# Kernel tuning notes

Hardware: AMD Instinct MI355X
Metric: run time of the kernel (lower is better)

## Reference

```python
import jax, jax.numpy as jnp
import numpy as np

N = 50000  # nodes per ntype (must be equal across ntypes per the module's forward)
E = 400000  # edges per relation

# relation order matches __init__: (src_ntype, dst_ntype)
RELS = [("stock","financial"),("stock","macro"),("stock","news"),("stock","policy"),
        ("financial","macro"),("financial","stock"),("financial","news"),("financial","policy"),
        ("macro","stock"),("macro","financial"),("macro","news"),("macro","policy"),
        ("news","stock"),("news","financial"),("news","macro"),("news","policy"),
        ("policy","stock"),("policy","macro"),("policy","news"),("policy","financial")]
NTYPES = ["stock","financial","macro","news","policy"]


def graph_conv(x_src, src, dst, W, b):
    # DGL GraphConv, norm='both': h = D_in^{-1/2} A D_out^{-1/2} x W + b
    ones = jnp.ones((src.shape[0],), x_src.dtype)
    deg_out = jax.ops.segment_sum(ones, src, num_segments=N)
    norm_s = jax.lax.rsqrt(jnp.maximum(deg_out, 1.0))
    h = x_src * norm_s[:, None]
    if W.shape[0] > W.shape[1]:  # mult W first when in_feats > out_feats
        h = h @ W
        agg = jax.ops.segment_sum(h[src], dst, num_segments=N)
    else:
        agg = jax.ops.segment_sum(h[src], dst, num_segments=N)
        agg = agg @ W
    deg_in = jax.ops.segment_sum(ones, dst, num_segments=N)
    norm_d = jax.lax.rsqrt(jnp.maximum(deg_in, 1.0))
    return agg * norm_d[:, None] + b


def hetero_layer(feats, edges, W_per_rel, b_per_rel):
    # sum-aggregate per destination ntype (aggregate='sum')
    out = {nt: jnp.zeros((N, b_per_rel[0].shape[0]), jnp.float32) for nt in NTYPES}
    for r, (s_nt, d_nt) in enumerate(RELS):
        out[d_nt] = out[d_nt] + graph_conv(feats[s_nt], edges[r, 0], edges[r, 1], W_per_rel[r], b_per_rel[r])
    return out


def setup_inputs() -> dict:
    key = jax.random.key(0)
    ks = jax.random.split(key, 16)
    H, C = 128, 10
    d = {
        "x_stock": jax.random.normal(ks[0], (N, 5), jnp.float32),
        "x_financial": jax.random.normal(ks[1], (N, 16), jnp.float32),
        "x_macro": jax.random.normal(ks[2], (N, 21), jnp.float32),
        "x_news": jax.random.normal(ks[3], (N, 768), jnp.float32),
        "x_policy": jax.random.normal(ks[4], (N, 768), jnp.float32),
        "W1_stock": jax.random.normal(ks[5], (4, 5, H), jnp.float32) * 0.1,
        "W1_financial": jax.random.normal(ks[6], (4, 16, H), jnp.float32) * 0.1,
        "W1_macro": jax.random.normal(ks[7], (4, 21, H), jnp.float32) * 0.1,
        "W1_news": jax.random.normal(ks[8], (4, 768, H), jnp.float32) * 0.02,
        "W1_policy": jax.random.normal(ks[9], (4, 768, H), jnp.float32) * 0.02,
        "b1": jnp.zeros((20, H), jnp.float32),
        "W2": jax.random.normal(ks[10], (20, H, H), jnp.float32) * 0.05,
        "b2": jnp.zeros((20, H), jnp.float32),
        "Wfc": jax.random.normal(ks[11], (H, C), jnp.float32) * 0.05,
        "bfc": jnp.zeros((C,), jnp.float32),
        "edges": jax.random.randint(ks[12], (20, 2, E), 0, N, dtype=jnp.int32),
    }
    return d


def reference(x_stock, x_financial, x_macro, x_news, x_policy,
              W1_stock, W1_financial, W1_macro, W1_news, W1_policy, b1,
              W2, b2, Wfc, bfc, edges):
    feats = {"stock": x_stock, "financial": x_financial, "macro": x_macro,
             "news": x_news, "policy": x_policy}
    # layer-1 weights in relation order (RELS grouped by src ntype, 4 each)
    W1_by_src = {"stock": W1_stock, "financial": W1_financial, "macro": W1_macro,
                 "news": W1_news, "policy": W1_policy}
    W1_list = [W1_by_src[s][r % 4] for r, (s, _) in enumerate(RELS)]
    b1_list = [b1[r] for r in range(20)]
    h1 = hetero_layer(feats, edges, W1_list, b1_list)
    W2_list = [W2[r] for r in range(20)]
    b2_list = [b2[r] for r in range(20)]
    h2 = hetero_layer(h1, edges, W2_list, b2_list)
    # manual cross-ntype accumulation into stock buffer, then divide by #ntypes
    acc = h2["stock"]
    for nt in NTYPES:
        if nt != "stock":
            acc = acc + h2[nt]
    acc = acc / len(NTYPES)
    # dgl.mean_nodes over a single graph -> [1, H]
    m = jnp.mean(acc, axis=0, keepdims=True)
    out = m @ Wfc + bfc
    return (m, out)
```

## Files before the change

kernel.cpp:

```cpp
#include <hip/hip_runtime.h>

#define NN 50000
#define EE 400000

#define CH_H 32768
#define NCH_H 2
#define ESL_H 2
#define EPS_H (EE/ESL_H)
#define I4_H (EPS_H/4)

#define ESL_C 4
#define EPS_C (EE/ESL_C)
#define I4_C (EPS_C/4)

#define CH_D 4096
#define NCH_D 13
#define ESL_D 2
#define EPS_D (EE/ESL_D)
#define I4_D (EPS_D/4)

#define NZ 261
#define ZROWS 192

#define VCH 96

__constant__ int DSTT[20]     = {1,2,3,4, 2,0,3,4, 0,1,3,4, 0,1,2,4, 0,2,3,1};
__constant__ int KIDX[20]     = {0,0,0,0, 1,0,1,1, 1,1,2,2, 2,2,2,3, 3,3,3,3};
__constant__ int DSTREL[5][4] = {{5,8,12,16},{0,9,13,19},{1,4,14,17},{2,6,10,18},{3,7,11,15}};
__constant__ int FEATS[5]     = {5, 16, 21, 768, 768};

#define OFF_HIST 0
#define OFF_CRAW 0
#define OFF_CC4  0
#define OFF_C    4000000
#define OFF_ND   5000000
#define OFF_PART 0
#define OFF_YS   6500000
#define OFF_S    6600000
#define OFF_V    6700000
#define OFF_NS   7000000
#define OFF_DACC 8000000
#define DSLICE   4000000
#define OFF_Y    8000000
#define OFF_MP   8110000
#define TOTAL_ELEMS 16000000

static __device__ __forceinline__ void fma4(float4& a, const float4& x, float w) {
    a.x += w * x.x; a.y += w * x.y; a.z += w * x.z; a.w += w * x.w;
}

__global__ __launch_bounds__(1024) void k_hist(const int* __restrict__ edges, int* __restrict__ hist_part) {
    __shared__ int h[CH_H];
    const int slice = blockIdx.x, chunk = blockIdx.y;
    const int r = blockIdx.z % 20, arr = blockIdx.z / 20;
    for (int i = threadIdx.x; i < CH_H; i += 1024) h[i] = 0;
    __syncthreads();
    const int4* key = (const int4*)(edges + (size_t)(r*2 + arr)*EE + slice*EPS_H);
    const int base = chunk * CH_H;
    for (int i = threadIdx.x; i < I4_H; i += 1024) {
        int4 k4 = key[i];
        unsigned a = (unsigned)(k4.x - base), b = (unsigned)(k4.y - base);
        unsigned c = (unsigned)(k4.z - base), d = (unsigned)(k4.w - base);
        if (a < CH_H) atomicAdd(&h[a], 1);
        if (b < CH_H) atomicAdd(&h[b], 1);
        if (c < CH_H) atomicAdd(&h[c], 1);
        if (d < CH_H) atomicAdd(&h[d], 1);
    }
    __syncthreads();
    int* outp = hist_part + (arr*ESL_H + slice)*1000000 + r*NN;
    for (int i = threadIdx.x; i < CH_H; i += 1024) {
        int u = base + i;
        if (u < NN) outp[u] = h[i];
    }
}

__global__ __launch_bounds__(256) void k_norms(const int* __restrict__ hist_part,
                                               float* __restrict__ ns, float* __restrict__ nd) {
    int r = blockIdx.y;
    int u = blockIdx.x * 256 + threadIdx.x;
    if (u >= NN) return;
    int idx = r*NN + u;
    float dop = (float)(hist_part[idx] + hist_part[1000000 + idx]);
    float dip = (float)(hist_part[2000000 + idx] + hist_part[3000000 + idx]);
    if (dop < 1.f) dop = 1.f;
    if (dip < 1.f) dip = 1.f;
    ns[idx] = 1.0f / sqrtf(dop);
    nd[idx] = 1.0f / sqrtf(dip);
}

__global__ __launch_bounds__(1024) void k_craw(const int* __restrict__ edges,
                                               const float* __restrict__ nd, float* __restrict__ craw_part) {
    __shared__ float h[CH_H];
    const int slice = blockIdx.x, chunk = blockIdx.y, r = blockIdx.z;
    for (int i = threadIdx.x; i < CH_H; i += 1024) h[i] = 0.f;
    __syncthreads();
    const int4* s4 = (const int4*)(edges + (size_t)(r*2)*EE + slice*EPS_C);
    const int4* d4 = (const int4*)(edges + (size_t)(r*2+1)*EE + slice*EPS_C);
    const float* ndr = nd + r*NN;
    const int base = chunk * CH_H;
    for (int i = threadIdx.x; i < I4_C; i += 1024) {
        int4 s = s4[i];
        int4 d = d4[i];
        unsigned a = (unsigned)(s.x - base), b = (unsigned)(s.y - base);
        unsigned c = (unsigned)(s.z - base), e = (unsigned)(s.w - base);
        if (a < CH_H) atomicAdd(&h[a], ndr[d.x]);
        if (b < CH_H) atomicAdd(&h[b], ndr[d.y]);
        if (c < CH_H) atomicAdd(&h[c], ndr[d.z]);
        if (e < CH_H) atomicAdd(&h[e], ndr[d.w]);
    }
    __syncthreads();
    float* outp = craw_part + slice*1000000 + r*NN;
    for (int i = threadIdx.x; i < CH_H; i += 1024) {
        int u = base + i;
        if (u < NN) outp[u] = h[i];
    }
}

__global__ __launch_bounds__(256) void k_cS(const float* __restrict__ craw_part, const float* __restrict__ ns,
                                            float* __restrict__ c, float* __restrict__ S) {
    int r = blockIdx.y;
    int u = blockIdx.x * 256 + threadIdx.x;
    float val = 0.f;
    if (u < NN) {
        int idx = r*NN + u;
        val = ns[idx] * (craw_part[idx] + craw_part[1000000 + idx]
                       + craw_part[2000000 + idx] + craw_part[3000000 + idx]);
        c[idx] = val;
    }
    for (int off = 32; off > 0; off >>= 1) val += __shfl_down(val, off, 64);
    __shared__ float red[4];
    if ((threadIdx.x & 63) == 0) red[threadIdx.x >> 6] = val;
    __syncthreads();
    if (threadIdx.x == 0) atomicAdd(&S[r], red[0] + red[1] + red[2] + red[3]);
}

__global__ __launch_bounds__(256) void k_cc(const float* __restrict__ c, const float* __restrict__ nd,
                                            float* __restrict__ cc4) {
    int r1 = blockIdx.y;
    int u = blockIdx.x * 256 + threadIdx.x;
    if (u >= NN) return;
    float ndv = nd[r1*NN + u];
    int d1 = DSTT[r1];
    float4 w;
    w.x = c[(4*d1+0)*NN + u] * ndv;
    w.y = c[(4*d1+1)*NN + u] * ndv;
    w.z = c[(4*d1+2)*NN + u] * ndv;
    w.w = c[(4*d1+3)*NN + u] * ndv;
    *(float4*)(cc4 + (size_t)(r1*NN + u) * 4) = w;
}

__global__ __launch_bounds__(1024) void k_dacc(const int* __restrict__ edges,
                                               const float* __restrict__ cc4, float* __restrict__ dacc_part) {
    __shared__ float h4[CH_D * 4];
    const int slice = blockIdx.x, chunk = blockIdx.y, r = blockIdx.z;
    for (int i = threadIdx.x; i < CH_D * 4; i += 1024) h4[i] = 0.f;
    __syncthreads();
    const int4* s4 = (const int4*)(edges + (size_t)(r*2)*EE + slice*EPS_D);
    const int4* d4 = (const int4*)(edges + (size_t)(r*2+1)*EE + slice*EPS_D);
    const float* ccr = cc4 + (size_t)r*NN*4;
    const int base = chunk * CH_D;
    for (int i = threadIdx.x; i < I4_D; i += 1024) {
        int4 s = s4[i];
        int4 d = d4[i];
        unsigned a = (unsigned)(s.x - base), b = (unsigned)(s.y - base);
        unsigned c = (unsigned)(s.z - base), e = (unsigned)(s.w - base);
        if (a < CH_D) {
            const float4 w = *(const float4*)(ccr + (size_t)d.x * 4);
            atomicAdd(&h4[a*4+0], w.x); atomicAdd(&h4[a*4+1], w.y);
            atomicAdd(&h4[a*4+2], w.z); atomicAdd(&h4[a*4+3], w.w);
        }
        if (b < CH_D) {
            const float4 w = *(const float4*)(ccr + (size_t)d.y * 4);
            atomicAdd(&h4[b*4+0], w.x); atomicAdd(&h4[b*4+1], w.y);
            atomicAdd(&h4[b*4+2], w.z); atomicAdd(&h4[b*4+3], w.w);
        }
        if (c < CH_D) {
            const float4 w = *(const float4*)(ccr + (size_t)d.z * 4);
            atomicAdd(&h4[c*4+0], w.x); atomicAdd(&h4[c*4+1], w.y);
            atomicAdd(&h4[c*4+2], w.z); atomicAdd(&h4[c*4+3], w.w);
        }
        if (e < CH_D) {
            const float4 w = *(const float4*)(ccr + (size_t)d.w * 4);
            atomicAdd(&h4[e*4+0], w.x); atomicAdd(&h4[e*4+1], w.y);
            atomicAdd(&h4[e*4+2], w.z); atomicAdd(&h4[e*4+3], w.w);
        }
    }
    __syncthreads();
    const int d1 = DSTT[r], kk = KIDX[r];
    float* op = dacc_part + slice * DSLICE;
#pragma unroll
    for (int j = 0; j < 4; ++j) {
        int p = 4*(4*d1 + j) + kk;
        float* pj = op + (size_t)p*NN;
        for (int i = threadIdx.x; i < CH_D; i += 1024) {
            int u = base + i;
            if (u < NN) pj[u] = h4[i*4 + j];
        }
    }
}

__global__ __launch_bounds__(192) void k_y_big(const float* __restrict__ xn, const float* __restrict__ xp,
        const float* __restrict__ ns, const float* __restrict__ dacc, float* __restrict__ partial) {
    __shared__ float wlds[64 * 16];
    const int tid = threadIdx.x;
    const int z = blockIdx.x, group = blockIdx.y;
    const int s1 = 3 + group;
    const float* x = (group == 0) ? xn : xp;
    const int c0 = tid * 4;
    float4 acc[16];
#pragma unroll
    for (int q = 0; q < 16; ++q) acc[q] = make_float4(0.f, 0.f, 0.f, 0.f);

    for (int t = 0; t < 3; ++t) {
        const int u0 = z * ZROWS + t * 64;
        __syncthreads();
        for (int tt = tid; tt < 1024; tt += 192) {
            int ql = tt >> 6, ri = tt & 63;
            int i = ql >> 2, j = ql & 3;
            int r1 = 4*s1 + i;
            int p = 4*(4*DSTT[r1] + j) + KIDX[r1];
            int u = u0 + ri;
            float w = 0.f;
            if (u < NN) {
                int idx = p*NN + u;
                w = ns[r1*NN + u] * (dacc[idx] + dacc[DSLICE + idx]);
            }
            wlds[ri*16 + ql] = w;
        }
        __syncthreads();
        const int rmax = (NN - u0 < 64) ? (NN - u0) : 64;
#pragma unroll 4
        for (int ri = 0; ri < rmax; ++ri) {
            const float4 xv = *(const float4*)(x + (size_t)(u0 + ri) * 768 + c0);
            const float4 wa = *(const float4*)(wlds + ri * 16);
            const float4 wb = *(const float4*)(wlds + ri * 16 + 4);
            const float4 wc = *(const float4*)(wlds + ri * 16 + 8);
            const float4 wd = *(const float4*)(wlds + ri * 16 + 12);
            fma4(acc[0],  xv, wa.x); fma4(acc[1],  xv, wa.y);
            fma4(acc[2],  xv, wa.z); fma4(acc[3],  xv, wa.w);
            fma4(acc[4],  xv, wb.x); fma4(acc[5],  xv, wb.y);
            fma4(acc[6],  xv, wb.z); fma4(acc[7],  xv, wb.w);
            fma4(acc[8],  xv, wc.x); fma4(acc[9],  xv, wc.y);
            fma4(acc[10], xv, wc.z); fma4(acc[11], xv, wc.w);
            fma4(acc[12], xv, wd.x); fma4(acc[13], xv, wd.y);
            fma4(acc[14], xv, wd.z); fma4(acc[15], xv, wd.w);
        }
    }
    float* pslot = partial + (size_t)(z*2 + group) * 12288;
#pragma unroll
    for (int ql = 0; ql < 16; ++ql)
        *(float4*)(pslot + ql * 768 + c0) = acc[ql];
}

template<int F>
__global__ __launch_bounds__(256) void k_y_small(const float* __restrict__ x,
        const float* __restrict__ ns, const float* __restrict__ dacc,
        float* __restrict__ ys, int s1) {
    const int q = blockIdx.x;
    const int i = q >> 2, j = q & 3;
    const int r1 = 4*s1 + i;
    const int p = 4*(4*DSTT[r1] + j) + KIDX[r1];
    const float* nsp = ns + r1*NN;
    const float* d0 = dacc + (size_t)p*NN;
    const float* d1 = d0 + DSLICE;
    float acc[F];
#pragma unroll
    for (int f = 0; f < F; ++f) acc[f] = 0.f;
    const int u0 = blockIdx.y * 6250;
    for (int u = u0 + threadIdx.x; u < u0 + 6250; u += 256) {
        float w = nsp[u] * (d0[u] + d1[u]);
        const float* xr = x + (size_t)u * F;
#pragma unroll
        for (int f = 0; f < F; ++f) acc[f] += w * xr[f];
    }
#pragma unroll
    for (int f = 0; f < F; ++f)
        for (int off = 32; off > 0; off >>= 1) acc[f] += __shfl_down(acc[f], off, 64);
    __shared__ float red[F];
    if (threadIdx.x < F) red[threadIdx.x] = 0.f;
    __syncthreads();
    if ((threadIdx.x & 63) == 0) {
#pragma unroll
        for (int f = 0; f < F; ++f) atomicAdd(&red[f], acc[f]);
    }
    __syncthreads();
    if (threadIdx.x < F) atomicAdd(&ys[p*768 + threadIdx.x], red[threadIdx.x]);
}

__global__ __launch_bounds__(768) void k_red_y(const float* __restrict__ partial,
                                               const float* __restrict__ ys, float* __restrict__ y) {
    const int p = blockIdx.x;
    const int f = threadIdx.x;
    const int r2 = p >> 2, k = p & 3;
    const int r1 = DSTREL[r2 >> 2][k];
    const int s1 = r1 >> 2;
    float s = ys[p*768 + f];
    if (s1 >= 3) {
        const int group = s1 - 3;
        const int i = r1 & 3;
        const int ql = i * 4 + (r2 & 3);
        const float* base = partial + (size_t)group * 12288 + ql * 768 + f;
        for (int z = 0; z < NZ; ++z) s += base[(size_t)z * 2 * 12288];
    }
    y[p*768 + f] = s;
}

__global__ __launch_bounds__(128) void k_v(const float* __restrict__ y,
        const float* __restrict__ W1s, const float* __restrict__ W1f, const float* __restrict__ W1m,
        const float* __restrict__ W1n, const float* __restrict__ W1p, float* __restrict__ v) {
    const int r2 = blockIdx.x;
    const int k  = blockIdx.y;
    const int fc = blockIdx.z;
    const int c  = threadIdx.x;
    const int r1 = DSTREL[r2 >> 2][k];
    const int s1 = r1 >> 2;
    const int F  = FEATS[s1];
    const int f0 = fc * VCH;
    if (f0 >= F) return;
    const int f1 = (f0 + VCH < F) ? (f0 + VCH) : F;
    const float* W1 = (s1 == 0 ? W1s : s1 == 1 ? W1f : s1 == 2 ? W1m : s1 == 3 ? W1n : W1p)
                      + (size_t)(r1 & 3) * F * 128;
    const float* yp = y + (r2*4 + k) * 768;
    float sum = 0.f;
#pragma unroll 4
    for (int f = f0; f < f1; ++f) sum += yp[f] * W1[(size_t)f * 128 + c];
    atomicAdd(&v[r2 * 128 + c], sum);
}

__global__ __launch_bounds__(128) void k_m(const float* __restrict__ v, const float* __restrict__ S,
        const float* __restrict__ b1, const float* __restrict__ W2, float* __restrict__ mpart) {
    int r2 = blockIdx.x;
    int c = threadIdx.x;
    __shared__ float vp[128];
    int s2 = r2 >> 2;
    float b = b1[DSTREL[s2][0]*128 + c] + b1[DSTREL[s2][1]*128 + c]
            + b1[DSTREL[s2][2]*128 + c] + b1[DSTREL[s2][3]*128 + c];
    vp[c] = v[r2*128 + c] + S[r2] * b;
    __syncthreads();
    const float* W2r = W2 + r2 * 16384;
    float sum = 0.f;
    for (int k = 0; k < 128; ++k) sum += vp[k] * W2r[k * 128 + c];
    mpart[r2 * 128 + c] = sum;
}

__global__ __launch_bounds__(128) void k_out(const float* __restrict__ mpart, const float* __restrict__ b2,
        const float* __restrict__ Wfc, const float* __restrict__ bfc, float* __restrict__ out) {
    int c = threadIdx.x;
    __shared__ float ml[128];
    float bs = 0.f, ms = 0.f;
    for (int r2 = 0; r2 < 20; ++r2) { bs += b2[r2 * 128 + c]; ms += mpart[r2 * 128 + c]; }
    float m = (ms + (float)NN * bs) * (1.0f / (5.0f * (float)NN));
    out[c] = m;
    ml[c] = m;
    __syncthreads();
    if (c < 10) {
        float o = bfc[c];
        for (int k = 0; k < 128; ++k) o += ml[k] * Wfc[k * 10 + c];
        out[128 + c] = o;
    }
}

extern "C" void kernel_launch(void* const* d_in, const int* in_sizes, int n_in,
                              void* d_out, int out_size, void* d_ws, size_t ws_size,
                              hipStream_t stream) {
    (void)in_sizes; (void)n_in; (void)out_size;
    const float* xs  = (const float*)d_in[0];
    const float* xf  = (const float*)d_in[1];
    const float* xm  = (const float*)d_in[2];
    const float* xn  = (const float*)d_in[3];
    const float* xp  = (const float*)d_in[4];
    const float* W1s = (const float*)d_in[5];
    const float* W1f = (const float*)d_in[6];
    const float* W1m = (const float*)d_in[7];
    const float* W1n = (const float*)d_in[8];
    const float* W1p = (const float*)d_in[9];
    const float* b1  = (const float*)d_in[10];
    const float* W2  = (const float*)d_in[11];
    const float* b2  = (const float*)d_in[12];
    const float* Wfc = (const float*)d_in[13];
    const float* bfc = (const float*)d_in[14];
    const int* edges = (const int*)d_in[15];
    float* ws = (float*)d_ws;
    int* wsi = (int*)d_ws;
    float* out = (float*)d_out;
    if (ws_size < (size_t)TOTAL_ELEMS * 4) return;

    dim3 t256(256), nb(196, 20);

    hipMemsetAsync(ws + OFF_YS, 0, (size_t)(OFF_S + 64 - OFF_YS) * 4, stream);
    hipMemsetAsync(ws + OFF_V, 0, 2560 * 4, stream);

    k_hist<<<dim3(ESL_H, NCH_H, 40), dim3(1024), 0, stream>>>(edges, wsi + OFF_HIST);
    k_norms<<<nb, t256, 0, stream>>>(wsi + OFF_HIST, ws + OFF_NS, ws + OFF_ND);
    k_craw<<<dim3(ESL_C, NCH_H, 20), dim3(1024), 0, stream>>>(edges, ws + OFF_ND, ws + OFF_CRAW);
    k_cS<<<nb, t256, 0, stream>>>(ws + OFF_CRAW, ws + OFF_NS, ws + OFF_C, ws + OFF_S);
    k_cc<<<nb, t256, 0, stream>>>(ws + OFF_C, ws + OFF_ND, ws + OFF_CC4);
    k_dacc<<<dim3(ESL_D, NCH_D, 20), dim3(1024), 0, stream>>>(edges, ws + OFF_CC4, ws + OFF_DACC);
    k_y_big<<<dim3(NZ, 2), dim3(192), 0, stream>>>(xn, xp, ws + OFF_NS, ws + OFF_DACC, ws + OFF_PART);
    k_y_small<5><<<dim3(16, 8), t256, 0, stream>>>(xs, ws + OFF_NS, ws + OFF_DACC, ws + OFF_YS, 0);
    k_y_small<16><<<dim3(16, 8), t256, 0, stream>>>(xf, ws + OFF_NS, ws + OFF_DACC, ws + OFF_YS, 1);
    k_y_small<21><<<dim3(16, 8), t256, 0, stream>>>(xm, ws + OFF_NS, ws + OFF_DACC, ws + OFF_YS, 2);
    k_red_y<<<dim3(80), dim3(768), 0, stream>>>(ws + OFF_PART, ws + OFF_YS, ws + OFF_Y);
    k_v<<<dim3(20, 4, 8), dim3(128), 0, stream>>>(ws + OFF_Y, W1s, W1f, W1m, W1n, W1p, ws + OFF_V);
    k_m<<<dim3(20), dim3(128), 0, stream>>>(ws + OFF_V, ws + OFF_S, b1, W2, ws + OFF_MP);
    k_out<<<dim3(1), dim3(128), 0, stream>>>(ws + OFF_MP, b2, Wfc, bfc, out);
}
```

Baseline: 944.4 us.

## Double-buffer k_y_big weight staging, merge k_y_small j-loops, retile k_dacc

Three changes. k_y_big now prefetches the next 64-row weight tile into registers while computing on the current one, using two LDS buffers so the global gather overlaps the FMA loop. k_y_small processes all four j outputs per block, so x is read once instead of four times. k_dacc uses larger chunks (5056 nodes, 10 chunks, about 80 KB of LDS) with a flattened block index, which cuts redundant edge scans but lowers occupancy per CU.

```diff
diff --git a/kernel.cpp b/kernel.cpp
--- a/kernel.cpp
+++ b/kernel.cpp
@@ -13,8 +13,8 @@
 #define EPS_C (EE/ESL_C)
 #define I4_C (EPS_C/4)
 
-#define CH_D 4096
-#define NCH_D 13
+#define CH_D 5056
+#define NCH_D 10
 #define ESL_D 2
 #define EPS_D (EE/ESL_D)
 #define I4_D (EPS_D/4)
@@ -152,7 +152,10 @@
 __global__ __launch_bounds__(1024) void k_dacc(const int* __restrict__ edges,
                                                const float* __restrict__ cc4, float* __restrict__ dacc_part) {
     __shared__ float h4[CH_D * 4];
-    const int slice = blockIdx.x, chunk = blockIdx.y, r = blockIdx.z;
+    const int bid = blockIdx.x;
+    const int sp = bid % 40;
+    const int chunk = bid / 40;
+    const int slice = sp / 20, r = sp % 20;
     for (int i = threadIdx.x; i < CH_D * 4; i += 1024) h4[i] = 0.f;
     __syncthreads();
     const int4* s4 = (const int4*)(edges + (size_t)(r*2)*EE + slice*EPS_D);
@@ -201,50 +204,78 @@
 
 __global__ __launch_bounds__(192) void k_y_big(const float* __restrict__ xn, const float* __restrict__ xp,
         const float* __restrict__ ns, const float* __restrict__ dacc, float* __restrict__ partial) {
-    __shared__ float wlds[64 * 16];
+    __shared__ __align__(16) float wlds[2][64 * 16];
     const int tid = threadIdx.x;
     const int z = blockIdx.x, group = blockIdx.y;
     const int s1 = 3 + group;
     const float* x = (group == 0) ? xn : xp;
     const int c0 = tid * 4;
-    float4 acc[16];
-#pragma unroll
-    for (int q = 0; q < 16; ++q) acc[q] = make_float4(0.f, 0.f, 0.f, 0.f);
-
-    for (int t = 0; t < 3; ++t) {
-        const int u0 = z * ZROWS + t * 64;
-        __syncthreads();
-        for (int tt = tid; tt < 1024; tt += 192) {
+
+    int pp[6], rr[6], rim[6];
+#pragma unroll
+    for (int k = 0; k < 6; ++k) {
+        int tt = tid + k * 192;
+        if (tt < 1024) {
             int ql = tt >> 6, ri = tt & 63;
             int i = ql >> 2, j = ql & 3;
             int r1 = 4*s1 + i;
-            int p = 4*(4*DSTT[r1] + j) + KIDX[r1];
-            int u = u0 + ri;
+            pp[k] = 4*(4*DSTT[r1] + j) + KIDX[r1];
+            rr[k] = r1;
+            rim[k] = ri;
+        } else pp[k] = -1;
+    }
+
+    float4 acc[16];
+#pragma unroll
+    for (int q = 0; q < 16; ++q) acc[q] = make_float4(0.f, 0.f, 0.f, 0.f);
+    float stage[6];
+
+    auto fill = [&](int t) {
+        const int u0 = z * ZROWS + t * 64;
+#pragma unroll
+        for (int k = 0; k < 6; ++k) {
             float w = 0.f;
-            if (u < NN) {
-                int idx = p*NN + u;
-                w = ns[r1*NN + u] * (dacc[idx] + dacc[DSLICE + idx]);
+            if (pp[k] >= 0) {
+                int u = u0 + rim[k];
+                if (u < NN) {
+                    int idx = pp[k]*NN + u;
+                    w = ns[rr[k]*NN + u] * (dacc[idx] + dacc[DSLICE + idx]);
+                }
             }
-            wlds[ri*16 + ql] = w;
-        }
-        __syncthreads();
+            stage[k] = w;
+        }
+    };
+    auto store = [&](int buf) {
+#pragma unroll
+        for (int k = 0; k < 6; ++k) {
+            int tt = tid + k * 192;
+            if (tt < 1024) wlds[buf][(tt & 63)*16 + (tt >> 6)] = stage[k];
+        }
+    };
+
+    fill(0); store(0); __syncthreads();
+    for (int t = 0; t < 3; ++t) {
+        if (t < 2) fill(t + 1);
+        const int u0 = z * ZROWS + t * 64;
         const int rmax = (NN - u0 < 64) ? (NN - u0) : 64;
+        const float* wb = wlds[t & 1];
 #pragma unroll 4
         for (int ri = 0; ri < rmax; ++ri) {
             const float4 xv = *(const float4*)(x + (size_t)(u0 + ri) * 768 + c0);
-            const float4 wa = *(const float4*)(wlds + ri * 16);
-            const float4 wb = *(const float4*)(wlds + ri * 16 + 4);
-            const float4 wc = *(const float4*)(wlds + ri * 16 + 8);
-            const float4 wd = *(const float4*)(wlds + ri * 16 + 12);
-            fma4(acc[0],  xv, wa.x); fma4(acc[1],  xv, wa.y);
-            fma4(acc[2],  xv, wa.z); fma4(acc[3],  xv, wa.w);
-            fma4(acc[4],  xv, wb.x); fma4(acc[5],  xv, wb.y);
-            fma4(acc[6],  xv, wb.z); fma4(acc[7],  xv, wb.w);
-            fma4(acc[8],  xv, wc.x); fma4(acc[9],  xv, wc.y);
-            fma4(acc[10], xv, wc.z); fma4(acc[11], xv, wc.w);
-            fma4(acc[12], xv, wd.x); fma4(acc[13], xv, wd.y);
-            fma4(acc[14], xv, wd.z); fma4(acc[15], xv, wd.w);
-        }
+            const float4 wa = *(const float4*)(wb + ri * 16);
+            const float4 wbv = *(const float4*)(wb + ri * 16 + 4);
+            const float4 wc = *(const float4*)(wb + ri * 16 + 8);
+            const float4 wd = *(const float4*)(wb + ri * 16 + 12);
+            fma4(acc[0],  xv, wa.x);  fma4(acc[1],  xv, wa.y);
+            fma4(acc[2],  xv, wa.z);  fma4(acc[3],  xv, wa.w);
+            fma4(acc[4],  xv, wbv.x); fma4(acc[5],  xv, wbv.y);
+            fma4(acc[6],  xv, wbv.z); fma4(acc[7],  xv, wbv.w);
+            fma4(acc[8],  xv, wc.x);  fma4(acc[9],  xv, wc.y);
+            fma4(acc[10], xv, wc.z);  fma4(acc[11], xv, wc.w);
+            fma4(acc[12], xv, wd.x);  fma4(acc[13], xv, wd.y);
+            fma4(acc[14], xv, wd.z);  fma4(acc[15], xv, wd.w);
+        }
+        if (t < 2) { store((t + 1) & 1); __syncthreads(); }
     }
     float* pslot = partial + (size_t)(z*2 + group) * 12288;
 #pragma unroll
@@ -256,35 +287,55 @@
 __global__ __launch_bounds__(256) void k_y_small(const float* __restrict__ x,
         const float* __restrict__ ns, const float* __restrict__ dacc,
         float* __restrict__ ys, int s1) {
-    const int q = blockIdx.x;
-    const int i = q >> 2, j = q & 3;
+    const int i = blockIdx.x;
     const int r1 = 4*s1 + i;
-    const int p = 4*(4*DSTT[r1] + j) + KIDX[r1];
     const float* nsp = ns + r1*NN;
-    const float* d0 = dacc + (size_t)p*NN;
-    const float* d1 = d0 + DSLICE;
-    float acc[F];
-#pragma unroll
-    for (int f = 0; f < F; ++f) acc[f] = 0.f;
+    const float* d0[4]; const float* d1[4];
+#pragma unroll
+    for (int j = 0; j < 4; ++j) {
+        int p = 4*(4*DSTT[r1] + j) + KIDX[r1];
+        d0[j] = dacc + (size_t)p*NN;
+        d1[j] = d0[j] + DSLICE;
+    }
+    float acc[4][F];
+#pragma unroll
+    for (int j = 0; j < 4; ++j)
+#pragma unroll
+        for (int f = 0; f < F; ++f) acc[j][f] = 0.f;
     const int u0 = blockIdx.y * 6250;
     for (int u = u0 + threadIdx.x; u < u0 + 6250; u += 256) {
-        float w = nsp[u] * (d0[u] + d1[u]);
+        float nsv = nsp[u];
+        float w[4];
+#pragma unroll
+        for (int j = 0; j < 4; ++j) w[j] = nsv * (d0[j][u] + d1[j][u]);
         const float* xr = x + (size_t)u * F;
 #pragma unroll
-        for (int f = 0; f < F; ++f) acc[f] += w * xr[f];
-    }
-#pragma unroll
-    for (int f = 0; f < F; ++f)
-        for (int off = 32; off > 0; off >>= 1) acc[f] += __shfl_down(acc[f], off, 64);
-    __shared__ float red[F];
-    if (threadIdx.x < F) red[threadIdx.x] = 0.f;
+        for (int f = 0; f < F; ++f) {
+            float xv = xr[f];
+#pragma unroll
+            for (int j = 0; j < 4; ++j) acc[j][f] += w[j] * xv;
+        }
+    }
+#pragma unroll
+    for (int j = 0; j < 4; ++j)
+#pragma unroll
+        for (int f = 0; f < F; ++f)
+            for (int off = 32; off > 0; off >>= 1) acc[j][f] += __shfl_down(acc[j][f], off, 64);
+    __shared__ float red[4 * F];
+    if (threadIdx.x < 4 * F) red[threadIdx.x] = 0.f;
     __syncthreads();
     if ((threadIdx.x & 63) == 0) {
 #pragma unroll
-        for (int f = 0; f < F; ++f) atomicAdd(&red[f], acc[f]);
-    }
-    __syncthreads();
-    if (threadIdx.x < F) atomicAdd(&ys[p*768 + threadIdx.x], red[threadIdx.x]);
+        for (int j = 0; j < 4; ++j)
+#pragma unroll
+            for (int f = 0; f < F; ++f) atomicAdd(&red[j*F + f], acc[j][f]);
+    }
+    __syncthreads();
+    if (threadIdx.x < 4 * F) {
+        int j = threadIdx.x / F, f = threadIdx.x % F;
+        int p = 4*(4*DSTT[r1] + j) + KIDX[r1];
+        atomicAdd(&ys[p*768 + f], red[threadIdx.x]);
+    }
 }
 
 __global__ __launch_bounds__(768) void k_red_y(const float* __restrict__ partial,
@@ -395,11 +446,11 @@
     k_craw<<<dim3(ESL_C, NCH_H, 20), dim3(1024), 0, stream>>>(edges, ws + OFF_ND, ws + OFF_CRAW);
     k_cS<<<nb, t256, 0, stream>>>(ws + OFF_CRAW, ws + OFF_NS, ws + OFF_C, ws + OFF_S);
     k_cc<<<nb, t256, 0, stream>>>(ws + OFF_C, ws + OFF_ND, ws + OFF_CC4);
-    k_dacc<<<dim3(ESL_D, NCH_D, 20), dim3(1024), 0, stream>>>(edges, ws + OFF_CC4, ws + OFF_DACC);
+    k_dacc<<<dim3(40 * NCH_D), dim3(1024), 0, stream>>>(edges, ws + OFF_CC4, ws + OFF_DACC);
     k_y_big<<<dim3(NZ, 2), dim3(192), 0, stream>>>(xn, xp, ws + OFF_NS, ws + OFF_DACC, ws + OFF_PART);
-    k_y_small<5><<<dim3(16, 8), t256, 0, stream>>>(xs, ws + OFF_NS, ws + OFF_DACC, ws + OFF_YS, 0);
-    k_y_small<16><<<dim3(16, 8), t256, 0, stream>>>(xf, ws + OFF_NS, ws + OFF_DACC, ws + OFF_YS, 1);
-    k_y_small<21><<<dim3(16, 8), t256, 0, stream>>>(xm, ws + OFF_NS, ws + OFF_DACC, ws + OFF_YS, 2);
+    k_y_small<5><<<dim3(4, 8), t256, 0, stream>>>(xs, ws + OFF_NS, ws + OFF_DACC, ws + OFF_YS, 0);
+    k_y_small<16><<<dim3(4, 8), t256, 0, stream>>>(xf, ws + OFF_NS, ws + OFF_DACC, ws + OFF_YS, 1);
+    k_y_small<21><<<dim3(4, 8), t256, 0, stream>>>(xm, ws + OFF_NS, ws + OFF_DACC, ws + OFF_YS, 2);
     k_red_y<<<dim3(80), dim3(768), 0, stream>>>(ws + OFF_PART, ws + OFF_YS, ws + OFF_Y);
     k_v<<<dim3(20, 4, 8), dim3(128), 0, stream>>>(ws + OFF_Y, W1s, W1f, W1m, W1n, W1p, ws + OFF_V);
     k_m<<<dim3(20), dim3(128), 0, stream>>>(ws + OFF_V, ws + OFF_S, b1, W2, ws + OFF_MP);
```

After: 986.5 us. 1.04x slower.
